# Kernel tuning notes

Measured on AMD Instinct MI355X. Metric: run time of the kernel, lower is better.

## Reference

```python
import jax, jax.numpy as jnp
import numpy as np

BSZ, SEQ, EMBED = 2, 4096, 1024
NUM_HEADS = 16
HEAD_DIM = EMBED // NUM_HEADS
WINDOW = 256  # attention_window[layer_id]


def setup_inputs() -> dict:
    key = jax.random.key(0)
    ks = jax.random.split(key, 7)
    s = 1.0 / np.sqrt(EMBED)
    return {
        "hidden_states": jax.random.normal(ks[0], (BSZ, SEQ, EMBED), jnp.float32),
        "Wq": jax.random.normal(ks[1], (EMBED, EMBED), jnp.float32) * s,
        "bq": jnp.zeros((EMBED,), jnp.float32),
        "Wk": jax.random.normal(ks[2], (EMBED, EMBED), jnp.float32) * s,
        "bk": jnp.zeros((EMBED,), jnp.float32),
        "Wv": jax.random.normal(ks[3], (EMBED, EMBED), jnp.float32) * s,
        "bv": jnp.zeros((EMBED,), jnp.float32),
    }


def _blocks3(x, nb, w):
    # x: [b, s + 2w, h, d] -> [b, nb, 3w, h, d]; block c sees key blocks c-1, c, c+1
    b = x.shape[0]
    xb = x.reshape(b, nb + 2, w, NUM_HEADS, HEAD_DIM)
    return jnp.concatenate([xb[:, i:i + nb] for i in range(3)], axis=2)


def reference(hidden_states, Wq, bq, Wk, bk, Wv, bv):
    b, s, e = hidden_states.shape
    w = WINDOW
    nb = s // w
    q = (hidden_states @ Wq + bq) * (1.0 / np.sqrt(HEAD_DIM))
    k = hidden_states @ Wk + bk
    v = hidden_states @ Wv + bv
    q = q.reshape(b, nb, w, NUM_HEADS, HEAD_DIM)
    k = k.reshape(b, s, NUM_HEADS, HEAD_DIM)
    v = v.reshape(b, s, NUM_HEADS, HEAD_DIM)
    pad = ((0, 0), (w, w), (0, 0), (0, 0))
    kb = _blocks3(jnp.pad(k, pad), nb, w)  # [b, nb, 3w, h, d]
    vb = _blocks3(jnp.pad(v, pad), nb, w)
    # banded scores: query x in block n attends keys at global pos n*w - w + y
    scores = jnp.einsum('bnxhd,bnyhd->bnhxy', q, kb)  # [b, nb, h, w, 3w]
    x_idx = jnp.arange(w)
    y_idx = jnp.arange(3 * w)
    band = jnp.abs(y_idx[None, :] - x_idx[:, None] - w) <= w  # [w, 3w]
    kpos = jnp.arange(nb)[:, None] * w - w + y_idx[None, :]   # [nb, 3w]
    inb = (kpos >= 0) & (kpos < s)
    mask = band[None, :, :] & inb[:, None, :]                 # [nb, w, 3w]
    scores = jnp.where(mask[None, :, None, :, :], scores, -jnp.inf)
    probs = jax.nn.softmax(scores.astype(jnp.float32), axis=-1).astype(v.dtype)
    attn = jnp.einsum('bnhxy,bnyhd->bnxhd', probs, vb)        # [b, nb, w, h, d]
    return attn.reshape(b, s, e)
```

## Files before the change

kernel.cpp:

```cpp
#include <hip/hip_runtime.h>
#include <stdint.h>

#define SEQ    4096
#define EMBED  1024
#define NHEAD  16
#define HDIM   64
#define WIN    256
#define BSZ    2
#define M_TOT  (BSZ * SEQ)
#define N_QKV  3072
#define N_QK   2048
#define K_DIM  1024
#define LOG2E  1.4426950408889634f

typedef __attribute__((ext_vector_type(8))) __bf16 bf16x8;
typedef __attribute__((ext_vector_type(4))) float  f32x4;

__device__ __forceinline__ unsigned short f2bf(float f) {
  union { float f; unsigned int u; } c; c.f = f;
  unsigned int u = c.u;
  unsigned int r = (u + 0x7FFFu + ((u >> 16) & 1u)) >> 16;
  return (unsigned short)r;
}

__device__ __forceinline__ unsigned int cvt_pk_bf16(float lo, float hi) {
  unsigned int r;
  asm("v_cvt_pk_bf16_f32 %0, %1, %2" : "=v"(r) : "v"(lo), "v"(hi));
  return r;
}

__device__ __forceinline__ void gl2lds16(const void* g, void* l) {
  __builtin_amdgcn_global_load_lds((const __attribute__((address_space(1))) void*)g,
                                   (__attribute__((address_space(3))) void*)l, 16, 0, 0);
}

__global__ __launch_bounds__(256) void cvt_h(const float* __restrict__ in,
                                             unsigned short* __restrict__ out) {
  int i = (blockIdx.x * 256 + threadIdx.x) * 4;
  float4 v = *(const float4*)(in + i);
  ushort4 o;
  o.x = f2bf(v.x); o.y = f2bf(v.y); o.z = f2bf(v.z); o.w = f2bf(v.w);
  *(ushort4*)(out + i) = o;
}

__global__ __launch_bounds__(256) void cvt_w(const float* __restrict__ Wq,
                                             const float* __restrict__ Wk,
                                             const float* __restrict__ Wv,
                                             unsigned short* __restrict__ Wt) {
  __shared__ float t[32][33];
  int z = blockIdx.z;
  const float* W = (z == 0) ? Wq : (z == 1) ? Wk : Wv;
  int kb = blockIdx.x * 32, nb = blockIdx.y * 32;
  int tx = threadIdx.x, ty = threadIdx.y;
  for (int it = 0; it < 4; ++it) {
    int k = kb + ty + it * 8;
    t[ty + it * 8][tx] = W[(size_t)k * 1024 + nb + tx];
  }
  __syncthreads();
  for (int it = 0; it < 4; ++it) {
    int n = nb + ty + it * 8;
    Wt[(size_t)(z * 1024 + n) * 1024 + kb + tx] = f2bf(t[tx][ty + it * 8]);
  }
}

__global__ __launch_bounds__(512, 2) void qkv_gemm(const unsigned short* __restrict__ A,
                                                   const unsigned short* __restrict__ Bt,
                                                   const float* __restrict__ bq,
                                                   const float* __restrict__ bk,
                                                   const float* __restrict__ bv,
                                                   unsigned short* __restrict__ C,
                                                   unsigned short* __restrict__ Vt) {
  __shared__ unsigned short As[2][256 * 64];
  __shared__ unsigned short Bs[2][256 * 64];
  int tid  = threadIdx.x;
  int lane = tid & 63, wave = tid >> 6;
  int ln   = lane & 15, quad = lane >> 4;
  int flat = blockIdx.y * 12 + blockIdx.x;
  int swz  = (flat & 7) * 48 + (flat >> 3);
  int m0 = (swz / 12) * 256, n0 = (swz % 12) * 256;
  int wy = wave >> 2, wx = wave & 3;
  f32x4 acc[8][4];
#pragma unroll
  for (int i = 0; i < 8; ++i)
#pragma unroll
    for (int j = 0; j < 4; ++j) acc[i][j] = (f32x4){0.f, 0.f, 0.f, 0.f};

  int c8 = tid & 7;
  int aR[2][2], bR[2][2];
#pragma unroll
  for (int s = 0; s < 2; ++s) {
    int rir = s * 64 + (tid >> 3);
    int la = (rir & 63) | ((rir & 64) << 1);
    int lb = (rir & 31) | ((rir >> 5) << 6);
    aR[0][s] = la;  aR[1][s] = la + 64;
    bR[0][s] = lb;  bR[1][s] = lb + 32;
  }

#define STG_A(buf, half, kt)                                                     \
  do {                                                                           \
    _Pragma("unroll")                                                            \
    for (int s = 0; s < 2; ++s) {                                                \
      int lr = aR[half][s]; int cg = c8 ^ (lr & 7);                              \
      gl2lds16(A + (size_t)(m0 + lr) * K_DIM + (kt) * 64 + cg * 8,               \
               &As[buf][lr * 64 + c8 * 8]);                                      \
    }                                                                            \
  } while (0)
#define STG_B(buf, half, kt)                                                     \
  do {                                                                           \
    _Pragma("unroll")                                                            \
    for (int s = 0; s < 2; ++s) {                                                \
      int lr = bR[half][s]; int cg = c8 ^ (lr & 7);                              \
      gl2lds16(Bt + (size_t)(n0 + lr) * K_DIM + (kt) * 64 + cg * 8,              \
               &Bs[buf][lr * 64 + c8 * 8]);                                      \
    }                                                                            \
  } while (0)

  STG_A(0, 0, 0); STG_B(0, 0, 0); STG_B(0, 1, 0); STG_A(0, 1, 0);
  STG_A(1, 0, 1); STG_B(1, 0, 1); STG_B(1, 1, 1);
  asm volatile("s_waitcnt vmcnt(6)" ::: "memory");
  __builtin_amdgcn_s_barrier();

  bf16x8 af[4][2], bv0[2][2], bv1[2][2];
  int aBase = wy * 128, bBase = wx * 64;

#pragma unroll 1
  for (int t = 0; t < 16; ++t) {
    int cur = t & 1;
    const unsigned short* as = As[cur];
    const unsigned short* bs = Bs[cur];

#pragma unroll
    for (int i2 = 0; i2 < 4; ++i2) {
      int row = aBase + i2 * 16 + ln;
#pragma unroll
      for (int ks = 0; ks < 2; ++ks) {
        int c = (ks * 4 + quad) ^ (row & 7);
        af[i2][ks] = *(const bf16x8*)&as[row * 64 + c * 8];
      }
    }
#pragma unroll
    for (int j2 = 0; j2 < 2; ++j2) {
      int row = bBase + j2 * 16 + ln;
#pragma unroll
      for (int ks = 0; ks < 2; ++ks) {
        int c = (ks * 4 + quad) ^ (row & 7);
        bv0[j2][ks] = *(const bf16x8*)&bs[row * 64 + c * 8];
      }
    }
    if (t < 15) STG_A(cur ^ 1, 1, t + 1);
    __builtin_amdgcn_s_barrier();
    __builtin_amdgcn_s_setprio(1);
#pragma unroll
    for (int ks = 0; ks < 2; ++ks)
#pragma unroll
      for (int i2 = 0; i2 < 4; ++i2)
#pragma unroll
        for (int j2 = 0; j2 < 2; ++j2)
          acc[i2][j2] = __builtin_amdgcn_mfma_f32_16x16x32_bf16(af[i2][ks], bv0[j2][ks], acc[i2][j2], 0, 0, 0);
    __builtin_amdgcn_s_setprio(0);
    __builtin_amdgcn_s_barrier();

#pragma unroll
    for (int j2 = 0; j2 < 2; ++j2) {
      int row = bBase + 32 + j2 * 16 + ln;
#pragma unroll
      for (int ks = 0; ks < 2; ++ks) {
        int c = (ks * 4 + quad) ^ (row & 7);
        bv1[j2][ks] = *(const bf16x8*)&bs[row * 64 + c * 8];
      }
    }
    if (t < 14) STG_A(cur, 0, t + 2);
    __builtin_amdgcn_s_barrier();
    __builtin_amdgcn_s_setprio(1);
#pragma unroll
    for (int ks = 0; ks < 2; ++ks)
#pragma unroll
      for (int i2 = 0; i2 < 4; ++i2)
#pragma unroll
        for (int j2 = 0; j2 < 2; ++j2)
          acc[i2][2 + j2] = __builtin_amdgcn_mfma_f32_16x16x32_bf16(af[i2][ks], bv1[j2][ks], acc[i2][2 + j2], 0, 0, 0);
    __builtin_amdgcn_s_setprio(0);
    __builtin_amdgcn_s_barrier();

#pragma unroll
    for (int i2 = 0; i2 < 4; ++i2) {
      int row = aBase + 64 + i2 * 16 + ln;
#pragma unroll
      for (int ks = 0; ks < 2; ++ks) {
        int c = (ks * 4 + quad) ^ (row & 7);
        af[i2][ks] = *(const bf16x8*)&as[row * 64 + c * 8];
      }
    }
    if (t < 14) STG_B(cur, 0, t + 2);
    __builtin_amdgcn_s_barrier();
    __builtin_amdgcn_s_setprio(1);
#pragma unroll
    for (int ks = 0; ks < 2; ++ks)
#pragma unroll
      for (int i2 = 0; i2 < 4; ++i2)
#pragma unroll
        for (int j2 = 0; j2 < 2; ++j2)
          acc[4 + i2][j2] = __builtin_amdgcn_mfma_f32_16x16x32_bf16(af[i2][ks], bv0[j2][ks], acc[4 + i2][j2], 0, 0, 0);
    __builtin_amdgcn_s_setprio(0);
    __builtin_amdgcn_s_barrier();

    if (t < 14) STG_B(cur, 1, t + 2);
    __builtin_amdgcn_s_barrier();
    __builtin_amdgcn_s_setprio(1);
#pragma unroll
    for (int ks = 0; ks < 2; ++ks)
#pragma unroll
      for (int i2 = 0; i2 < 4; ++i2)
#pragma unroll
        for (int j2 = 0; j2 < 2; ++j2)
          acc[4 + i2][2 + j2] = __builtin_amdgcn_mfma_f32_16x16x32_bf16(af[i2][ks], bv1[j2][ks], acc[4 + i2][2 + j2], 0, 0, 0);
    __builtin_amdgcn_s_setprio(0);
    asm volatile("s_waitcnt vmcnt(6)" ::: "memory");
    __builtin_amdgcn_s_barrier();
  }
#undef STG_A
#undef STG_B

  if (n0 < N_QK) {
#pragma unroll
    for (int j = 0; j < 4; ++j) {
      int n = n0 + wx * 64 + j * 16 + ln;
      float bias, scl;
      if (n < 1024) { bias = bq[n];        scl = 0.125f * LOG2E; }
      else          { bias = bk[n - 1024]; scl = 1.f; }
#pragma unroll
      for (int i = 0; i < 8; ++i) {
        int mb = m0 + wy * 128 + i * 16 + quad * 4;
#pragma unroll
        for (int r = 0; r < 4; ++r) {
          float v = (acc[i][j][r] + bias) * scl;
          C[(size_t)(mb + r) * N_QK + n] = f2bf(v);
        }
      }
    }
  } else {
#pragma unroll
    for (int j = 0; j < 4; ++j) {
      int n  = n0 + wx * 64 + j * 16 + ln;
      int hd = n - 2048;
      float bias = bv[hd];
#pragma unroll
      for (int i = 0; i < 8; ++i) {
        int mb  = m0 + wy * 128 + i * 16 + quad * 4;
        int bb  = mb >> 12;
        int pos = mb & (SEQ - 1);
        ushort4 pk;
        pk.x = f2bf(acc[i][j][0] + bias);
        pk.y = f2bf(acc[i][j][1] + bias);
        pk.z = f2bf(acc[i][j][2] + bias);
        pk.w = f2bf(acc[i][j][3] + bias);
        *(ushort4*)&Vt[((size_t)bb * (NHEAD * HDIM) + hd) * SEQ + pos] = pk;
      }
    }
  }
}

__global__ __launch_bounds__(256) void attn(const unsigned short* __restrict__ qk,
                                            const unsigned short* __restrict__ vtg,
                                            float* __restrict__ out) {
  __shared__ unsigned short Kl[64 * 72];
  __shared__ unsigned short Vl[64 * 72];
  int tid  = threadIdx.x;
  int lane = tid & 63, wave = tid >> 6;
  int ln   = lane & 15, quad = lane >> 4;
  int bx = blockIdx.x;
  int lx = ((bx & 7) << 3) | (bx >> 3);
  int q0 = lx * 64, head = blockIdx.y, b = blockIdx.z;
  size_t baseRow = (size_t)b * SEQ;
  const unsigned short* kptr = qk + 1024;
  const unsigned short* vrow = vtg + ((size_t)(b * NHEAD + head) * HDIM) * SEQ;

  int sy = tid >> 3, sc = tid & 7;
  const unsigned short* kbase = kptr + (baseRow + sy) * (size_t)N_QK + head * HDIM + sc * 8;
  const unsigned short* vbase = vrow + (size_t)sy * SEQ + sc * 8;

  bf16x8 qf[2];
  {
    size_t ro = (baseRow + q0 + wave * 16 + ln) * (size_t)N_QK + head * HDIM + quad * 8;
    qf[0] = *(const bf16x8*)&qk[ro];
    qf[1] = *(const bf16x8*)&qk[ro + 32];
  }

  float l_st = 0.f;
  f32x4 o_acc[4];
  for (int dt = 0; dt < 4; ++dt) o_acc[dt] = (f32x4){0.f, 0.f, 0.f, 0.f};

  int lo = (q0 >= 256) ? 0 : (256 - q0) / 64;
  int hi = (SEQ + 256 - q0) / 64; if (hi > 9) hi = 9;

  uint4 pk0, pk1, pv0, pv1;
#define PREFETCH(KT)                                                        \
  {                                                                         \
    pk0 = *(const uint4*)&kbase[(size_t)(KT) * N_QK];                       \
    pk1 = *(const uint4*)&kbase[(size_t)((KT) + 32) * N_QK];                \
    pv0 = *(const uint4*)&vbase[(KT)];                                      \
    pv1 = *(const uint4*)&vbase[(size_t)32 * SEQ + (KT)];                   \
  }

  PREFETCH(q0 - 256 + lo * 64);

  int srcA = ((lane & 16) << 1) | ln;
  int srcB = srcA + 16;
  bool hiQ = (lane & 32) != 0;

  for (int t = lo; t < hi; ++t) {
    int kt = q0 - 256 + t * 64;
    __syncthreads();
    *(uint4*)&Kl[sy * 72 + sc * 8]        = pk0;
    *(uint4*)&Kl[(sy + 32) * 72 + sc * 8] = pk1;
    *(uint4*)&Vl[sy * 72 + sc * 8]        = pv0;
    *(uint4*)&Vl[(sy + 32) * 72 + sc * 8] = pv1;
    __syncthreads();

    if (t + 1 < hi) { PREFETCH(kt + 64); }

    f32x4 s[4];
    __builtin_amdgcn_s_setprio(1);
    for (int nt = 0; nt < 4; ++nt) {
      bf16x8 kf0 = *(const bf16x8*)&Kl[(nt * 16 + ln) * 72 + quad * 8];
      bf16x8 kf1 = *(const bf16x8*)&Kl[(nt * 16 + ln) * 72 + 32 + quad * 8];
      f32x4 z = (f32x4){0.f, 0.f, 0.f, 0.f};
      z = __builtin_amdgcn_mfma_f32_16x16x32_bf16(kf0, qf[0], z, 0, 0, 0);
      z = __builtin_amdgcn_mfma_f32_16x16x32_bf16(kf1, qf[1], z, 0, 0, 0);
      s[nt] = z;
    }
    __builtin_amdgcn_s_setprio(0);

    if (t == 0 || t == 8) {
      int qq = q0 + wave * 16 + ln;
      for (int nt = 0; nt < 4; ++nt) {
        int kb = kt + nt * 16 + quad * 4 - qq;
        for (int r = 0; r < 4; ++r) {
          int dd = kb + r;
          if (dd < -WIN || dd > WIN) s[nt][r] = -INFINITY;
        }
      }
    }

    float rs = 0.f;
    for (int nt = 0; nt < 4; ++nt)
      for (int r = 0; r < 4; ++r) {
        float p = exp2f(s[nt][r]);
        s[nt][r] = p;
        rs += p;
      }
    l_st += rs;

    unsigned int p01[4], p23[4];
    for (int nt = 0; nt < 4; ++nt) {
      p01[nt] = cvt_pk_bf16(s[nt][0], s[nt][1]);
      p23[nt] = cvt_pk_bf16(s[nt][2], s[nt][3]);
    }

    for (int ks = 0; ks < 2; ++ks) {
      int ntA = 2 * ks, ntB = 2 * ks + 1;
      unsigned int a0 = (unsigned int)__shfl((int)p01[ntA], srcA);
      unsigned int a1 = (unsigned int)__shfl((int)p23[ntA], srcA);
      unsigned int a2 = (unsigned int)__shfl((int)p01[ntA], srcB);
      unsigned int a3 = (unsigned int)__shfl((int)p23[ntA], srcB);
      unsigned int b0 = (unsigned int)__shfl((int)p01[ntB], srcA);
      unsigned int b1 = (unsigned int)__shfl((int)p23[ntB], srcA);
      unsigned int b2 = (unsigned int)__shfl((int)p01[ntB], srcB);
      unsigned int b3 = (unsigned int)__shfl((int)p23[ntB], srcB);
      union { uint4 u; bf16x8 v; } pf;
      pf.u.x = hiQ ? b0 : a0;
      pf.u.y = hiQ ? b1 : a1;
      pf.u.z = hiQ ? b2 : a2;
      pf.u.w = hiQ ? b3 : a3;
      __builtin_amdgcn_s_setprio(1);
      for (int dt = 0; dt < 4; ++dt) {
        bf16x8 vf = *(const bf16x8*)&Vl[(dt * 16 + ln) * 72 + ks * 32 + quad * 8];
        o_acc[dt] = __builtin_amdgcn_mfma_f32_16x16x32_bf16(vf, pf.v, o_acc[dt], 0, 0, 0);
      }
      __builtin_amdgcn_s_setprio(0);
    }
  }

  float l = l_st;
  l += __shfl_xor(l, 16);
  l += __shfl_xor(l, 32);
  float inv = 1.0f / l;
  int qpos = q0 + wave * 16 + ln;
  float* ob = out + (baseRow + qpos) * (size_t)EMBED + head * HDIM + quad * 4;
  for (int dt = 0; dt < 4; ++dt) {
    float4 v;
    v.x = o_acc[dt][0] * inv;
    v.y = o_acc[dt][1] * inv;
    v.z = o_acc[dt][2] * inv;
    v.w = o_acc[dt][3] * inv;
    *(float4*)(ob + dt * 16) = v;
  }
#undef PREFETCH
}

extern "C" void kernel_launch(void* const* d_in, const int* in_sizes, int n_in,
                              void* d_out, int out_size, void* d_ws, size_t ws_size,
                              hipStream_t stream) {
  const float* h  = (const float*)d_in[0];
  const float* Wq = (const float*)d_in[1];
  const float* bq = (const float*)d_in[2];
  const float* Wk = (const float*)d_in[3];
  const float* bk = (const float*)d_in[4];
  const float* Wv = (const float*)d_in[5];
  const float* bv = (const float*)d_in[6];
  float* out = (float*)d_out;

  unsigned short* h_bf  = (unsigned short*)d_ws;
  unsigned short* wt_bf = h_bf + (size_t)M_TOT * K_DIM;
  unsigned short* qk    = wt_bf + (size_t)N_QKV * K_DIM;
  unsigned short* vtg   = qk + (size_t)M_TOT * N_QK;

  cvt_h<<<(M_TOT * K_DIM) / 1024, 256, 0, stream>>>(h, h_bf);
  cvt_w<<<dim3(32, 32, 3), dim3(32, 8), 0, stream>>>(Wq, Wk, Wv, wt_bf);
  qkv_gemm<<<dim3(12, 32), 512, 0, stream>>>(h_bf, wt_bf, bq, bk, bv, qk, vtg);
  attn<<<dim3(SEQ / 64, NHEAD, BSZ), 256, 0, stream>>>(qk, vtg, out);
}
```

Measured before the change: 214.5 us.

## Shrink QKV GEMM M-tile to 128 and merge conversion kernels

The QKV GEMM block tile drops from 256x256 to 128x256, so twice as many workgroups are launched (768 instead of 384). The main loop is restaged with two MFMA phases per k-step instead of four, and the A-tile LDS buffer is halved. The input and weight fp32-to-bf16 conversion kernels are merged into one launch to save a kernel launch. The smaller tile gives better occupancy and wave balance across CUs, at the cost of lower per-block data reuse and more B-matrix traffic. The diff also leaves a dead, immediately undefined set of macros.

```diff
diff --git a/kernel.cpp b/kernel.cpp
--- a/kernel.cpp
+++ b/kernel.cpp
@@ -34,32 +34,36 @@
                                    (__attribute__((address_space(3))) void*)l, 16, 0, 0);
 }
 
-__global__ __launch_bounds__(256) void cvt_h(const float* __restrict__ in,
-                                             unsigned short* __restrict__ out) {
-  int i = (blockIdx.x * 256 + threadIdx.x) * 4;
-  float4 v = *(const float4*)(in + i);
-  ushort4 o;
-  o.x = f2bf(v.x); o.y = f2bf(v.y); o.z = f2bf(v.z); o.w = f2bf(v.w);
-  *(ushort4*)(out + i) = o;
-}
-
-__global__ __launch_bounds__(256) void cvt_w(const float* __restrict__ Wq,
-                                             const float* __restrict__ Wk,
-                                             const float* __restrict__ Wv,
-                                             unsigned short* __restrict__ Wt) {
+__global__ __launch_bounds__(256) void cvt_all(const float* __restrict__ in,
+                                               unsigned short* __restrict__ out,
+                                               const float* __restrict__ Wq,
+                                               const float* __restrict__ Wk,
+                                               const float* __restrict__ Wv,
+                                               unsigned short* __restrict__ Wt) {
   __shared__ float t[32][33];
-  int z = blockIdx.z;
-  const float* W = (z == 0) ? Wq : (z == 1) ? Wk : Wv;
-  int kb = blockIdx.x * 32, nb = blockIdx.y * 32;
-  int tx = threadIdx.x, ty = threadIdx.y;
-  for (int it = 0; it < 4; ++it) {
-    int k = kb + ty + it * 8;
-    t[ty + it * 8][tx] = W[(size_t)k * 1024 + nb + tx];
-  }
-  __syncthreads();
-  for (int it = 0; it < 4; ++it) {
-    int n = nb + ty + it * 8;
-    Wt[(size_t)(z * 1024 + n) * 1024 + kb + tx] = f2bf(t[tx][ty + it * 8]);
+  int tid = threadIdx.x;
+  if (blockIdx.x < 8192) {
+    int i = (blockIdx.x * 256 + tid) * 4;
+    float4 v = *(const float4*)(in + i);
+    ushort4 o;
+    o.x = f2bf(v.x); o.y = f2bf(v.y); o.z = f2bf(v.z); o.w = f2bf(v.w);
+    *(ushort4*)(out + i) = o;
+  } else {
+    int wb = blockIdx.x - 8192;
+    int z  = wb >> 10;
+    int rem = wb & 1023;
+    int kb = (rem & 31) * 32, nb = (rem >> 5) * 32;
+    const float* W = (z == 0) ? Wq : (z == 1) ? Wk : Wv;
+    int tx = tid & 31, ty = tid >> 5;
+    for (int it = 0; it < 4; ++it) {
+      int k = kb + ty + it * 8;
+      t[ty + it * 8][tx] = W[(size_t)k * 1024 + nb + tx];
+    }
+    __syncthreads();
+    for (int it = 0; it < 4; ++it) {
+      int n = nb + ty + it * 8;
+      Wt[(size_t)(z * 1024 + n) * 1024 + kb + tx] = f2bf(t[tx][ty + it * 8]);
+    }
   }
 }
 
@@ -70,58 +74,92 @@
                                                    const float* __restrict__ bv,
                                                    unsigned short* __restrict__ C,
                                                    unsigned short* __restrict__ Vt) {
-  __shared__ unsigned short As[2][256 * 64];
+  __shared__ unsigned short As[2][128 * 64];
   __shared__ unsigned short Bs[2][256 * 64];
   int tid  = threadIdx.x;
   int lane = tid & 63, wave = tid >> 6;
   int ln   = lane & 15, quad = lane >> 4;
   int flat = blockIdx.y * 12 + blockIdx.x;
-  int swz  = (flat & 7) * 48 + (flat >> 3);
-  int m0 = (swz / 12) * 256, n0 = (swz % 12) * 256;
+  int swz  = (flat & 7) * 96 + (flat >> 3);
+  int m0 = (swz / 12) * 128, n0 = (swz % 12) * 256;
   int wy = wave >> 2, wx = wave & 3;
-  f32x4 acc[8][4];
-#pragma unroll
-  for (int i = 0; i < 8; ++i)
+  f32x4 acc[4][4];
+#pragma unroll
+  for (int i = 0; i < 4; ++i)
 #pragma unroll
     for (int j = 0; j < 4; ++j) acc[i][j] = (f32x4){0.f, 0.f, 0.f, 0.f};
 
   int c8 = tid & 7;
-  int aR[2][2], bR[2][2];
-#pragma unroll
-  for (int s = 0; s < 2; ++s) {
-    int rir = s * 64 + (tid >> 3);
-    int la = (rir & 63) | ((rir & 64) << 1);
-    int lb = (rir & 31) | ((rir >> 5) << 6);
-    aR[0][s] = la;  aR[1][s] = la + 64;
-    bR[0][s] = lb;  bR[1][s] = lb + 32;
-  }
-
-#define STG_A(buf, half, kt)                                                     \
-  do {                                                                           \
-    _Pragma("unroll")                                                            \
-    for (int s = 0; s < 2; ++s) {                                                \
-      int lr = aR[half][s]; int cg = c8 ^ (lr & 7);                              \
+  int sRow[2];
+#pragma unroll
+  for (int s = 0; s < 2; ++s) sRow[s] = s * 64 + (tid >> 3);
+
+#define STG_A(buf, kt)                                                           \
+  do {                                                                           \
+    _Pragma("unroll")                                                            \
+    for (int s = 0; s < 2; ++s) {                                                \
+      int lr = sRow[s]; int cg = c8 ^ (lr & 7);                                  \
+      gl2lds16(A + (size_t)(m0 + lr) * K_DIM + (kt) * 64 + cg * 8,               \
+               &As[buf][lr * 512 + c8 * 8]);                                     \
+    }                                                                            \
+  } while (0)
+#define STG_BLO(buf, kt)                                                         \
+  do {                                                                           \
+    _Pragma("unroll")                                                            \
+    for (int s = 0; s < 2; ++s) {                                                \
+      int lr = sRow[s]; int cg = c8 ^ (lr & 7);                                  \
+      gl2lds16(Bt + (size_t)(n0 + lr) * K_DIM + (kt) * 64 + cg * 8,              \
+               &Bs[buf][lr * 512 + c8 * 8]);                                     \
+    }                                                                            \
+  } while (0)
+#define STG_BHI(buf, kt)                                                         \
+  do {                                                                           \
+    _Pragma("unroll")                                                            \
+    for (int s = 0; s < 2; ++s) {                                                \
+      int lr = sRow[s]; int cg = c8 ^ (lr & 7);                                  \
+      gl2lds16(Bt + (size_t)(n0 + 128 + lr) * K_DIM + (kt) * 64 + cg * 8,        \
+               &Bs[buf][128 * 512 + lr * 512 + c8 * 8]);                         \
+    }                                                                            \
+  } while (0)
+
+#undef STG_A
+#undef STG_BLO
+#undef STG_BHI
+#define STG_A(buf, kt)                                                           \
+  do {                                                                           \
+    _Pragma("unroll")                                                            \
+    for (int s = 0; s < 2; ++s) {                                                \
+      int lr = sRow[s]; int cg = c8 ^ (lr & 7);                                  \
       gl2lds16(A + (size_t)(m0 + lr) * K_DIM + (kt) * 64 + cg * 8,               \
                &As[buf][lr * 64 + c8 * 8]);                                      \
     }                                                                            \
   } while (0)
-#define STG_B(buf, half, kt)                                                     \
-  do {                                                                           \
-    _Pragma("unroll")                                                            \
-    for (int s = 0; s < 2; ++s) {                                                \
-      int lr = bR[half][s]; int cg = c8 ^ (lr & 7);                              \
+#define STG_BLO(buf, kt)                                                         \
+  do {                                                                           \
+    _Pragma("unroll")                                                            \
+    for (int s = 0; s < 2; ++s) {                                                \
+      int lr = sRow[s]; int cg = c8 ^ (lr & 7);                                  \
       gl2lds16(Bt + (size_t)(n0 + lr) * K_DIM + (kt) * 64 + cg * 8,              \
                &Bs[buf][lr * 64 + c8 * 8]);                                      \
     }                                                                            \
   } while (0)
-
-  STG_A(0, 0, 0); STG_B(0, 0, 0); STG_B(0, 1, 0); STG_A(0, 1, 0);
-  STG_A(1, 0, 1); STG_B(1, 0, 1); STG_B(1, 1, 1);
-  asm volatile("s_waitcnt vmcnt(6)" ::: "memory");
+#define STG_BHI(buf, kt)                                                         \
+  do {                                                                           \
+    _Pragma("unroll")                                                            \
+    for (int s = 0; s < 2; ++s) {                                                \
+      int lr = sRow[s]; int cg = c8 ^ (lr & 7);                                  \
+      gl2lds16(Bt + (size_t)(n0 + 128 + lr) * K_DIM + (kt) * 64 + cg * 8,        \
+               &Bs[buf][(128 + lr) * 64 + c8 * 8]);                              \
+    }                                                                            \
+  } while (0)
+
+  STG_A(0, 0); STG_BLO(0, 0); STG_BHI(0, 0);
+  STG_A(1, 1); STG_BLO(1, 1);
+  asm volatile("s_waitcnt vmcnt(4)" ::: "memory");
   __builtin_amdgcn_s_barrier();
 
   bf16x8 af[4][2], bv0[2][2], bv1[2][2];
-  int aBase = wy * 128, bBase = wx * 64;
+  int aBase = wy * 64, bBase = wx * 64;
 
 #pragma unroll 1
   for (int t = 0; t < 16; ++t) {
@@ -147,7 +185,7 @@
         bv0[j2][ks] = *(const bf16x8*)&bs[row * 64 + c * 8];
       }
     }
-    if (t < 15) STG_A(cur ^ 1, 1, t + 1);
+    if (t < 15) STG_BHI(cur ^ 1, t + 1);
     __builtin_amdgcn_s_barrier();
     __builtin_amdgcn_s_setprio(1);
 #pragma unroll
@@ -169,7 +207,7 @@
         bv1[j2][ks] = *(const bf16x8*)&bs[row * 64 + c * 8];
       }
     }
-    if (t < 14) STG_A(cur, 0, t + 2);
+    if (t < 14) { STG_A(cur, t + 2); STG_BLO(cur, t + 2); }
     __builtin_amdgcn_s_barrier();
     __builtin_amdgcn_s_setprio(1);
 #pragma unroll
@@ -180,46 +218,13 @@
         for (int j2 = 0; j2 < 2; ++j2)
           acc[i2][2 + j2] = __builtin_amdgcn_mfma_f32_16x16x32_bf16(af[i2][ks], bv1[j2][ks], acc[i2][2 + j2], 0, 0, 0);
     __builtin_amdgcn_s_setprio(0);
+    if (t < 14) asm volatile("s_waitcnt vmcnt(4)" ::: "memory");
+    else        asm volatile("s_waitcnt vmcnt(0)" ::: "memory");
     __builtin_amdgcn_s_barrier();
-
-#pragma unroll
-    for (int i2 = 0; i2 < 4; ++i2) {
-      int row = aBase + 64 + i2 * 16 + ln;
-#pragma unroll
-      for (int ks = 0; ks < 2; ++ks) {
-        int c = (ks * 4 + quad) ^ (row & 7);
-        af[i2][ks] = *(const bf16x8*)&as[row * 64 + c * 8];
-      }
-    }
-    if (t < 14) STG_B(cur, 0, t + 2);
-    __builtin_amdgcn_s_barrier();
-    __builtin_amdgcn_s_setprio(1);
-#pragma unroll
-    for (int ks = 0; ks < 2; ++ks)
-#pragma unroll
-      for (int i2 = 0; i2 < 4; ++i2)
-#pragma unroll
-        for (int j2 = 0; j2 < 2; ++j2)
-          acc[4 + i2][j2] = __builtin_amdgcn_mfma_f32_16x16x32_bf16(af[i2][ks], bv0[j2][ks], acc[4 + i2][j2], 0, 0, 0);
-    __builtin_amdgcn_s_setprio(0);
-    __builtin_amdgcn_s_barrier();
-
-    if (t < 14) STG_B(cur, 1, t + 2);
-    __builtin_amdgcn_s_barrier();
-    __builtin_amdgcn_s_setprio(1);
-#pragma unroll
-    for (int ks = 0; ks < 2; ++ks)
-#pragma unroll
-      for (int i2 = 0; i2 < 4; ++i2)
-#pragma unroll
-        for (int j2 = 0; j2 < 2; ++j2)
-          acc[4 + i2][2 + j2] = __builtin_amdgcn_mfma_f32_16x16x32_bf16(af[i2][ks], bv1[j2][ks], acc[4 + i2][2 + j2], 0, 0, 0);
-    __builtin_amdgcn_s_setprio(0);
-    asm volatile("s_waitcnt vmcnt(6)" ::: "memory");
-    __builtin_amdgcn_s_barrier();
   }
 #undef STG_A
-#undef STG_B
+#undef STG_BLO
+#undef STG_BHI
 
   if (n0 < N_QK) {
 #pragma unroll
@@ -229,8 +234,8 @@
       if (n < 1024) { bias = bq[n];        scl = 0.125f * LOG2E; }
       else          { bias = bk[n - 1024]; scl = 1.f; }
 #pragma unroll
-      for (int i = 0; i < 8; ++i) {
-        int mb = m0 + wy * 128 + i * 16 + quad * 4;
+      for (int i = 0; i < 4; ++i) {
+        int mb = m0 + wy * 64 + i * 16 + quad * 4;
 #pragma unroll
         for (int r = 0; r < 4; ++r) {
           float v = (acc[i][j][r] + bias) * scl;
@@ -245,8 +250,8 @@
       int hd = n - 2048;
       float bias = bv[hd];
 #pragma unroll
-      for (int i = 0; i < 8; ++i) {
-        int mb  = m0 + wy * 128 + i * 16 + quad * 4;
+      for (int i = 0; i < 4; ++i) {
+        int mb  = m0 + wy * 64 + i * 16 + quad * 4;
         int bb  = mb >> 12;
         int pos = mb & (SEQ - 1);
         ushort4 pk;
@@ -415,8 +420,7 @@
   unsigned short* qk    = wt_bf + (size_t)N_QKV * K_DIM;
   unsigned short* vtg   = qk + (size_t)M_TOT * N_QK;
 
-  cvt_h<<<(M_TOT * K_DIM) / 1024, 256, 0, stream>>>(h, h_bf);
-  cvt_w<<<dim3(32, 32, 3), dim3(32, 8), 0, stream>>>(Wq, Wk, Wv, wt_bf);
-  qkv_gemm<<<dim3(12, 32), 512, 0, stream>>>(h_bf, wt_bf, bq, bk, bv, qk, vtg);
+  cvt_all<<<8192 + 3072, 256, 0, stream>>>(h, h_bf, Wq, Wk, Wv, wt_bf);
+  qkv_gemm<<<dim3(12, 64), 512, 0, stream>>>(h_bf, wt_bf, bq, bk, bv, qk, vtg);
   attn<<<dim3(SEQ / 64, NHEAD, BSZ), 256, 0, stream>>>(qk, vtg, out);
 }
```

After: 207.3 us. 1.03x faster.
